# Optimization experiments

Measured on AMD Instinct MI355X. Metric: run time of the kernel, lower is better.

Reference implementation:

```python
import jax, jax.numpy as jnp
import numpy as np

F_BINS = 12
T_STEPS = 15
N = F_BINS * T_STEPS  # 180 patches
C = 768
R = C // 4            # 192 reduced dim for Q/K
B = 256
LN_EPS = 1e-5


def _build_physical_adjacency():
    A = np.zeros((N, N), dtype=np.float32)
    for f in range(F_BINS):
        for t in range(T_STEPS):
            i = f * T_STEPS + t
            if t < T_STEPS - 1:
                j = f * T_STEPS + (t + 1)
                A[i, j] = 1.0
                A[j, i] = 1.0
            hf = f * 2 + 1
            if hf < F_BINS:
                j = hf * T_STEPS + t
                A[i, j] = 1.0
                A[j, i] = 1.0
    A = A / (A.sum(axis=1, keepdims=True) + 1e-8)
    return jnp.asarray(A)


def setup_inputs() -> dict:
    key = jax.random.key(0)
    ks = jax.random.split(key, 8)
    x = jax.random.normal(ks[0], (B, N, C), dtype=jnp.float32)
    Wq = jax.random.normal(ks[1], (C, R), dtype=jnp.float32) * 0.02
    bq = jnp.zeros((R,), dtype=jnp.float32)
    Wk = jax.random.normal(ks[2], (C, R), dtype=jnp.float32) * 0.02
    bk = jnp.zeros((R,), dtype=jnp.float32)
    Wg = jax.random.normal(ks[3], (C, C), dtype=jnp.float32) * 0.02
    bg = jnp.zeros((C,), dtype=jnp.float32)
    gamma = jnp.ones((C,), dtype=jnp.float32)
    beta = jnp.zeros((C,), dtype=jnp.float32)
    alpha = jnp.asarray(0.8, dtype=jnp.float32)
    A_phys = _build_physical_adjacency()
    return {"x": x, "Wq": Wq, "bq": bq, "Wk": Wk, "bk": bk,
            "Wg": Wg, "bg": bg, "gamma": gamma, "beta": beta,
            "alpha": alpha, "A_phys": A_phys}


def reference(x, Wq, bq, Wk, bk, Wg, bg, gamma, beta, alpha, A_phys):
    # Q/K projections: [B,N,R]
    Q = jnp.einsum('bnc,cr->bnr', x, Wq) + bq
    K = jnp.einsum('bnc,cr->bnr', x, Wk) + bk
    # Dynamic adjacency: scaled dot-product softmax over nodes.
    scores = jnp.einsum('bnr,bmr->bnm', Q, K) / jnp.sqrt(jnp.asarray(R, x.dtype))
    A_dyn = jax.nn.softmax(scores, axis=-1)  # dropout is identity in eval
    a = jax.nn.sigmoid(alpha)
    A_comb = a * A_phys[None, :, :] + (1.0 - a) * A_dyn
    # GCN aggregation + projection
    z = jnp.einsum('bnm,bmc->bnc', A_comb, x)
    z = jnp.einsum('bnc,cd->bnd', z, Wg) + bg
    h = x + jax.nn.relu(z)
    # LayerNorm over channel dim
    mu = jnp.mean(h, axis=-1, keepdims=True)
    var = jnp.mean((h - mu) ** 2, axis=-1, keepdims=True)
    out = (h - mu) * jax.lax.rsqrt(var + LN_EPS) * gamma + beta
    return out
```

## Files before the change

kernel.cpp:

```cpp
#include <hip/hip_runtime.h>
#include <hip/hip_bf16.h>
#include <math.h>

#define BB   256
#define NN   180
#define CC   768
#define RR   192
#define MROWS (BB*NN)
#define KPAD 192

typedef __attribute__((ext_vector_type(8))) __bf16 bf16x8;
typedef __attribute__((ext_vector_type(4))) __bf16 bf16x4;
typedef __attribute__((ext_vector_type(4))) float  floatx4;

#define LDK 40

template<int MODE>
__global__ __launch_bounds__(256) void gemm_bt(
    const __bf16* __restrict__ A,  int lda, long sAb,
    const __bf16* __restrict__ Bt, int ldb, long sBb,
    void* __restrict__ Cout, int ldc, long sCb,
    int M, int N, int K,
    const float* __restrict__ bias,
    const float* __restrict__ scale,
    const float* __restrict__ addx)
{
    const int z = blockIdx.z;
    const __bf16* Ab = A  + (long)z * sAb;
    const __bf16* Bb = Bt + (long)z * sBb;
    const int m0 = blockIdx.y * 64;
    const int n0 = blockIdx.x * 64;
    const int t  = threadIdx.x;
    const int w  = t >> 6;
    const int l  = t & 63;
    const int lr = l & 15;
    const int q  = l >> 4;

    __shared__ __align__(16) __bf16 lds_a[64 * LDK];
    __shared__ __align__(16) __bf16 lds_b[64 * LDK];

    floatx4 acc[4] = {};

    const int srow = t >> 2;
    const int skc  = (t & 3) * 8;

    for (int k0 = 0; k0 < K; k0 += 32) {
        bf16x8 av = {};
        int am = m0 + srow;
        if (am < M) av = *reinterpret_cast<const bf16x8*>(Ab + (long)am * lda + k0 + skc);
        *reinterpret_cast<bf16x8*>(&lds_a[srow * LDK + skc]) = av;

        bf16x8 bv = {};
        int bn = n0 + srow;
        if (bn < N) bv = *reinterpret_cast<const bf16x8*>(Bb + (long)bn * ldb + k0 + skc);
        *reinterpret_cast<bf16x8*>(&lds_b[srow * LDK + skc]) = bv;

        __syncthreads();

        bf16x8 af = *reinterpret_cast<const bf16x8*>(&lds_a[(w * 16 + lr) * LDK + q * 8]);
#pragma unroll
        for (int s = 0; s < 4; ++s) {
            bf16x8 bfv = *reinterpret_cast<const bf16x8*>(&lds_b[(s * 16 + lr) * LDK + q * 8]);
            acc[s] = __builtin_amdgcn_mfma_f32_16x16x32_bf16(af, bfv, acc[s], 0, 0, 0);
        }
        __syncthreads();
    }

#pragma unroll
    for (int s = 0; s < 4; ++s) {
#pragma unroll
        for (int r = 0; r < 4; ++r) {
            int m = m0 + w * 16 + q * 4 + r;
            int n = n0 + s * 16 + lr;
            if (m < M && n < N) {
                float v = acc[s][r];
                if (MODE == 0) {
                    v = (v + bias[n]) * scale[n];
                    ((__bf16*)Cout)[(long)z * sCb + (long)m * ldc + n] = (__bf16)v;
                } else if (MODE == 1 || MODE == 2) {
                    ((__bf16*)Cout)[(long)z * sCb + (long)m * ldc + n] = (__bf16)v;
                } else {
                    v = v + bias[n];
                    v = v > 0.f ? v : 0.f;
                    v += addx[(long)m * ldc + n];
                    ((float*)Cout)[(long)m * ldc + n] = v;
                }
            }
        }
    }
}

__global__ __launch_bounds__(256) void convert_x(const float4* __restrict__ x4,
                                                 __bf16* __restrict__ xb, int n4)
{
    int i = blockIdx.x * 256 + threadIdx.x;
    int stride = gridDim.x * 256;
    for (; i < n4; i += stride) {
        float4 v = x4[i];
        bf16x4 o;
        o[0] = (__bf16)v.x; o[1] = (__bf16)v.y; o[2] = (__bf16)v.z; o[3] = (__bf16)v.w;
        *reinterpret_cast<bf16x4*>(xb + 4 * (long)i) = o;
    }
}

__global__ __launch_bounds__(256) void prep_weights(
    const float* __restrict__ Wq, const float* __restrict__ bq,
    const float* __restrict__ Wk, const float* __restrict__ bk,
    const float* __restrict__ Wg,
    __bf16* __restrict__ WqkT, __bf16* __restrict__ WgT,
    float* __restrict__ biasqk, float* __restrict__ scaleqk)
{
    int blk = blockIdx.x, t = threadIdx.x;
    if (blk < 384) {
        int n = blk;
        const float* W = (n < RR) ? Wq : Wk;
        int nn = (n < RR) ? n : n - RR;
        for (int k = t; k < CC; k += 256)
            WqkT[(long)n * CC + k] = (__bf16)W[(long)k * RR + nn];
        if (blk == 0) {
            for (int i = t; i < 384; i += 256) {
                biasqk[i]  = (i < RR) ? bq[i] : bk[i - RR];
                scaleqk[i] = (i < RR) ? rsqrtf((float)RR) : 1.0f;
            }
        }
    } else {
        int n = blk - 384;
        for (int k = t; k < CC; k += 256)
            WgT[(long)n * CC + k] = (__bf16)Wg[(long)k * CC + n];
    }
}

__global__ __launch_bounds__(256) void transpose_x(const __bf16* __restrict__ xb,
                                                   __bf16* __restrict__ xbT)
{
    const int c0 = (blockIdx.x % 12) * 64;
    const int b  = blockIdx.x / 12;
    __shared__ __bf16 lds[64 * 194];
    const int t = threadIdx.x;

    for (int i = 0; i < 45; ++i) {
        int idx = i * 256 + t;
        int m = idx >> 6, c = idx & 63;
        lds[c * 194 + m] = xb[((long)(b * NN + m)) * CC + c0 + c];
    }
    __syncthreads();
    for (int j = 0; j < 48; ++j) {
        int idx = j * 256 + t;
        int c = idx / KPAD, m = idx % KPAD;
        __bf16 v = (m < NN) ? lds[c * 194 + m] : (__bf16)0.0f;
        xbT[((long)(b * CC + c0 + c)) * KPAD + m] = v;
    }
}

__global__ __launch_bounds__(256) void softmax_combine(
    const __bf16* __restrict__ S, const float* __restrict__ A_phys,
    const float* __restrict__ alpha, __bf16* __restrict__ Acomb)
{
    const int w = threadIdx.x >> 6, l = threadIdx.x & 63;
    const long row = (long)blockIdx.x * 4 + w;
    const int b = (int)(row / NN), n = (int)(row % NN);
    const __bf16* Srow = S + ((long)b * NN + n) * NN;

    float v[3];
#pragma unroll
    for (int i = 0; i < 3; ++i) {
        int m = l + 64 * i;
        v[i] = (m < NN) ? (float)Srow[m] : -1e30f;
    }
    float mx = fmaxf(fmaxf(v[0], v[1]), v[2]);
    for (int off = 32; off; off >>= 1) mx = fmaxf(mx, __shfl_xor(mx, off, 64));

    float e[3], sum = 0.f;
#pragma unroll
    for (int i = 0; i < 3; ++i) {
        int m = l + 64 * i;
        e[i] = (m < NN) ? expf(v[i] - mx) : 0.f;
        sum += e[i];
    }
    for (int off = 32; off; off >>= 1) sum += __shfl_xor(sum, off, 64);

    const float a   = 1.f / (1.f + expf(-alpha[0]));
    const float inv = (1.f - a) / sum;
    __bf16* Orow = Acomb + ((long)b * NN + n) * KPAD;
#pragma unroll
    for (int i = 0; i < 3; ++i) {
        int m = l + 64 * i;
        if (m < KPAD) {
            float o = (m < NN) ? (a * A_phys[n * NN + m] + e[i] * inv) : 0.f;
            Orow[m] = (__bf16)o;
        }
    }
}

__global__ __launch_bounds__(256) void ln_kernel(float* __restrict__ out,
                                                 const float* __restrict__ gamma,
                                                 const float* __restrict__ beta)
{
    float* p = out + (long)blockIdx.x * CC;
    const int t = threadIdx.x, w = t >> 6, l = t & 63;
    float h[3], s = 0.f, s2 = 0.f;
#pragma unroll
    for (int i = 0; i < 3; ++i) {
        h[i] = p[t + 256 * i];
        s += h[i]; s2 += h[i] * h[i];
    }
    for (int off = 32; off; off >>= 1) { s += __shfl_xor(s, off, 64); s2 += __shfl_xor(s2, off, 64); }
    __shared__ float ps[4], ps2[4];
    if (l == 0) { ps[w] = s; ps2[w] = s2; }
    __syncthreads();
    s  = ps[0] + ps[1] + ps[2] + ps[3];
    s2 = ps2[0] + ps2[1] + ps2[2] + ps2[3];
    const float mu  = s * (1.f / CC);
    const float var = s2 * (1.f / CC) - mu * mu;
    const float rs  = rsqrtf(var + 1e-5f);
#pragma unroll
    for (int i = 0; i < 3; ++i) {
        int c = t + 256 * i;
        p[c] = (h[i] - mu) * rs * gamma[c] + beta[c];
    }
}

extern "C" void kernel_launch(void* const* d_in, const int* in_sizes, int n_in,
                              void* d_out, int out_size, void* d_ws, size_t ws_size,
                              hipStream_t stream)
{
    const float* x      = (const float*)d_in[0];
    const float* Wq     = (const float*)d_in[1];
    const float* bq     = (const float*)d_in[2];
    const float* Wk     = (const float*)d_in[3];
    const float* bk     = (const float*)d_in[4];
    const float* Wg     = (const float*)d_in[5];
    const float* bg     = (const float*)d_in[6];
    const float* gamma  = (const float*)d_in[7];
    const float* beta   = (const float*)d_in[8];
    const float* alpha  = (const float*)d_in[9];
    const float* A_phys = (const float*)d_in[10];

    char* w = (char*)d_ws;
    __bf16* xb    = (__bf16*)(w + 0);
    __bf16* zbuf  = xb;
    __bf16* xbT   = (__bf16*)(w + 70778880);
    __bf16* QK    = (__bf16*)(w + 146276352);
    __bf16* Acomb = QK;
    __bf16* S     = (__bf16*)(w + 181665792);
    __bf16* WqkT  = (__bf16*)(w + 198254592);
    __bf16* WgT   = (__bf16*)(w + 198844416);
    float*  biasqk  = (float*)(w + 200024064);
    float*  scaleqk = (float*)(w + 200025600);

    convert_x<<<4096, 256, 0, stream>>>((const float4*)x, xb, MROWS * CC / 4);
    prep_weights<<<384 + CC, 256, 0, stream>>>(Wq, bq, Wk, bk, Wg, WqkT, WgT, biasqk, scaleqk);
    transpose_x<<<BB * 12, 256, 0, stream>>>(xb, xbT);

    gemm_bt<0><<<dim3(384 / 64, MROWS / 64, 1), 256, 0, stream>>>(
        xb, CC, 0L, WqkT, CC, 0L, QK, 384, 0L,
        MROWS, 384, CC, biasqk, scaleqk, nullptr);

    gemm_bt<1><<<dim3(3, 3, BB), 256, 0, stream>>>(
        QK, 384, (long)NN * 384, QK + RR, 384, (long)NN * 384,
        S, NN, (long)NN * NN,
        NN, NN, RR, nullptr, nullptr, nullptr);

    softmax_combine<<<MROWS / 4, 256, 0, stream>>>(S, A_phys, alpha, Acomb);

    gemm_bt<2><<<dim3(CC / 64, 3, BB), 256, 0, stream>>>(
        Acomb, KPAD, (long)NN * KPAD, xbT, KPAD, (long)CC * KPAD,
        zbuf, CC, (long)NN * CC,
        NN, CC, KPAD, nullptr, nullptr, nullptr);

    gemm_bt<3><<<dim3(CC / 64, MROWS / 64, 1), 256, 0, stream>>>(
        zbuf, CC, 0L, WgT, CC, 0L, d_out, CC, 0L,
        MROWS, CC, CC, bg, nullptr, x);

    ln_kernel<<<MROWS, 256, 0, stream>>>((float*)d_out, gamma, beta);
}
```

Baseline: 760.4 us.

## Use 128x128 GEMM tiles with direct global-to-LDS loads

Replaces the 64x64 GEMM tile, where each wave held a 16x64 strip, with a 128x128 tile in which each wave computes a 64x64 sub-block of 4x4 MFMAs. Operands are loaded with global_load_lds straight into LDS, dropping the register round-trip, and out-of-range rows are clamped instead of zero-filled. The larger tile raises data reuse per LDS load and cuts global traffic for the big projection GEMMs. The trade-offs are more accumulator registers, an unpadded LDS layout that may cause bank conflicts, and more wasted work on the 180-row batched GEMMs.

```diff
diff --git a/kernel.cpp b/kernel.cpp
--- a/kernel.cpp
+++ b/kernel.cpp
@@ -1,6 +1,7 @@
 #include <hip/hip_runtime.h>
 #include <hip/hip_bf16.h>
 #include <math.h>
+#include <stdint.h>
 
 #define BB   256
 #define NN   180
@@ -13,10 +14,16 @@
 typedef __attribute__((ext_vector_type(4))) __bf16 bf16x4;
 typedef __attribute__((ext_vector_type(4))) float  floatx4;
 
-#define LDK 40
+__device__ __forceinline__ void gload_lds16(const __bf16* g, __bf16* lds)
+{
+    __builtin_amdgcn_global_load_lds(
+        (const __attribute__((address_space(1))) void*)(uintptr_t)(const void*)g,
+        (__attribute__((address_space(3))) void*)(uintptr_t)(void*)lds,
+        16, 0, 0);
+}
 
 template<int MODE>
-__global__ __launch_bounds__(256) void gemm_bt(
+__global__ __launch_bounds__(256) void gemm128(
     const __bf16* __restrict__ A,  int lda, long sAb,
     const __bf16* __restrict__ Bt, int ldb, long sBb,
     void* __restrict__ Cout, int ldc, long sCb,
@@ -28,62 +35,84 @@
     const int z = blockIdx.z;
     const __bf16* Ab = A  + (long)z * sAb;
     const __bf16* Bb = Bt + (long)z * sBb;
-    const int m0 = blockIdx.y * 64;
-    const int n0 = blockIdx.x * 64;
+    const int m0 = blockIdx.y * 128;
+    const int n0 = blockIdx.x * 128;
     const int t  = threadIdx.x;
     const int w  = t >> 6;
     const int l  = t & 63;
     const int lr = l & 15;
     const int q  = l >> 4;
 
-    __shared__ __align__(16) __bf16 lds_a[64 * LDK];
-    __shared__ __align__(16) __bf16 lds_b[64 * LDK];
-
-    floatx4 acc[4] = {};
-
-    const int srow = t >> 2;
-    const int skc  = (t & 3) * 8;
+    __shared__ __align__(16) __bf16 sa[128 * 32];
+    __shared__ __align__(16) __bf16 sb[128 * 32];
+
+    floatx4 acc[4][4] = {};
+
+    const int wm = (w & 1) * 64;
+    const int wn = (w >> 1) * 64;
+
+    const int srow = l >> 2;
+    const int skc  = (l & 3) * 8;
+
+    int arow0 = m0 + w * 16 + srow;        if (arow0 > M - 1) arow0 = M - 1;
+    int arow1 = m0 + (w + 4) * 16 + srow;  if (arow1 > M - 1) arow1 = M - 1;
+    int brow0 = n0 + w * 16 + srow;        if (brow0 > N - 1) brow0 = N - 1;
+    int brow1 = n0 + (w + 4) * 16 + srow;  if (brow1 > N - 1) brow1 = N - 1;
+
+    const __bf16* agp0 = Ab + (long)arow0 * lda + skc;
+    const __bf16* agp1 = Ab + (long)arow1 * lda + skc;
+    const __bf16* bgp0 = Bb + (long)brow0 * ldb + skc;
+    const __bf16* bgp1 = Bb + (long)brow1 * ldb + skc;
+
+    __bf16* sa0 = sa + (size_t)w * 512;
+    __bf16* sa1 = sa + (size_t)(w + 4) * 512;
+    __bf16* sb0 = sb + (size_t)w * 512;
+    __bf16* sb1 = sb + (size_t)(w + 4) * 512;
 
     for (int k0 = 0; k0 < K; k0 += 32) {
-        bf16x8 av = {};
-        int am = m0 + srow;
-        if (am < M) av = *reinterpret_cast<const bf16x8*>(Ab + (long)am * lda + k0 + skc);
-        *reinterpret_cast<bf16x8*>(&lds_a[srow * LDK + skc]) = av;
-
-        bf16x8 bv = {};
-        int bn = n0 + srow;
-        if (bn < N) bv = *reinterpret_cast<const bf16x8*>(Bb + (long)bn * ldb + k0 + skc);
-        *reinterpret_cast<bf16x8*>(&lds_b[srow * LDK + skc]) = bv;
-
+        gload_lds16(agp0 + k0, sa0);
+        gload_lds16(agp1 + k0, sa1);
+        gload_lds16(bgp0 + k0, sb0);
+        gload_lds16(bgp1 + k0, sb1);
         __syncthreads();
 
-        bf16x8 af = *reinterpret_cast<const bf16x8*>(&lds_a[(w * 16 + lr) * LDK + q * 8]);
-#pragma unroll
-        for (int s = 0; s < 4; ++s) {
-            bf16x8 bfv = *reinterpret_cast<const bf16x8*>(&lds_b[(s * 16 + lr) * LDK + q * 8]);
-            acc[s] = __builtin_amdgcn_mfma_f32_16x16x32_bf16(af, bfv, acc[s], 0, 0, 0);
-        }
+        bf16x8 af[4], bfv[4];
+#pragma unroll
+        for (int i = 0; i < 4; ++i)
+            af[i] = *reinterpret_cast<const bf16x8*>(&sa[(wm + i * 16 + lr) * 32 + q * 8]);
+#pragma unroll
+        for (int j = 0; j < 4; ++j)
+            bfv[j] = *reinterpret_cast<const bf16x8*>(&sb[(wn + j * 16 + lr) * 32 + q * 8]);
+#pragma unroll
+        for (int i = 0; i < 4; ++i)
+#pragma unroll
+            for (int j = 0; j < 4; ++j)
+                acc[i][j] = __builtin_amdgcn_mfma_f32_16x16x32_bf16(af[i], bfv[j], acc[i][j], 0, 0, 0);
         __syncthreads();
     }
 
 #pragma unroll
-    for (int s = 0; s < 4; ++s) {
-#pragma unroll
-        for (int r = 0; r < 4; ++r) {
-            int m = m0 + w * 16 + q * 4 + r;
-            int n = n0 + s * 16 + lr;
-            if (m < M && n < N) {
-                float v = acc[s][r];
-                if (MODE == 0) {
-                    v = (v + bias[n]) * scale[n];
-                    ((__bf16*)Cout)[(long)z * sCb + (long)m * ldc + n] = (__bf16)v;
-                } else if (MODE == 1 || MODE == 2) {
-                    ((__bf16*)Cout)[(long)z * sCb + (long)m * ldc + n] = (__bf16)v;
-                } else {
-                    v = v + bias[n];
-                    v = v > 0.f ? v : 0.f;
-                    v += addx[(long)m * ldc + n];
-                    ((float*)Cout)[(long)m * ldc + n] = v;
+    for (int i = 0; i < 4; ++i) {
+        const int mbase = m0 + wm + i * 16 + q * 4;
+#pragma unroll
+        for (int j = 0; j < 4; ++j) {
+            const int n = n0 + wn + j * 16 + lr;
+#pragma unroll
+            for (int r = 0; r < 4; ++r) {
+                const int m = mbase + r;
+                if (m < M && n < N) {
+                    float v = acc[i][j][r];
+                    if (MODE == 0) {
+                        v = (v + bias[n]) * scale[n];
+                        ((__bf16*)Cout)[(long)z * sCb + (long)m * ldc + n] = (__bf16)v;
+                    } else if (MODE == 1) {
+                        ((__bf16*)Cout)[(long)z * sCb + (long)m * ldc + n] = (__bf16)v;
+                    } else {
+                        v = v + bias[n];
+                        v = v > 0.f ? v : 0.f;
+                        v += addx[(long)m * ldc + n];
+                        ((float*)Cout)[(long)m * ldc + n] = v;
+                    }
                 }
             }
         }
@@ -252,23 +281,23 @@
     prep_weights<<<384 + CC, 256, 0, stream>>>(Wq, bq, Wk, bk, Wg, WqkT, WgT, biasqk, scaleqk);
     transpose_x<<<BB * 12, 256, 0, stream>>>(xb, xbT);
 
-    gemm_bt<0><<<dim3(384 / 64, MROWS / 64, 1), 256, 0, stream>>>(
+    gemm128<0><<<dim3(384 / 128, MROWS / 128, 1), 256, 0, stream>>>(
         xb, CC, 0L, WqkT, CC, 0L, QK, 384, 0L,
         MROWS, 384, CC, biasqk, scaleqk, nullptr);
 
-    gemm_bt<1><<<dim3(3, 3, BB), 256, 0, stream>>>(
+    gemm128<1><<<dim3(2, 2, BB), 256, 0, stream>>>(
         QK, 384, (long)NN * 384, QK + RR, 384, (long)NN * 384,
         S, NN, (long)NN * NN,
         NN, NN, RR, nullptr, nullptr, nullptr);
 
     softmax_combine<<<MROWS / 4, 256, 0, stream>>>(S, A_phys, alpha, Acomb);
 
-    gemm_bt<2><<<dim3(CC / 64, 3, BB), 256, 0, stream>>>(
+    gemm128<1><<<dim3(CC / 128, 2, BB), 256, 0, stream>>>(
         Acomb, KPAD, (long)NN * KPAD, xbT, KPAD, (long)CC * KPAD,
         zbuf, CC, (long)NN * CC,
         NN, CC, KPAD, nullptr, nullptr, nullptr);
 
-    gemm_bt<3><<<dim3(CC / 64, MROWS / 64, 1), 256, 0, stream>>>(
+    gemm128<3><<<dim3(CC / 128, MROWS / 128, 1), 256, 0, stream>>>(
         zbuf, CC, 0L, WgT, CC, 0L, d_out, CC, 0L,
         MROWS, CC, CC, bg, nullptr, x);
 
```

Result: faster. 701.6 us (-7.7%).
